# Kernel optimization log

Hardware: AMD Instinct MI355X
Metric: run time of the kernel (lower is better)

The kernel has to match this reference:

```python
import jax, jax.numpy as jnp
import numpy as np

DEGREE = 3
NUM_POINTS = 1024
EPS = 1e-5


def jacobi_kan(x, coeffs, a=1.0, b=1.0, degree=DEGREE):
    # x: (B, C_in, N) -> y: (B, C_out, N)
    t = jnp.tanh(jnp.transpose(x, (0, 2, 1)))  # (B, N, C_in)
    polys = [jnp.ones_like(t)]
    if degree > 0:
        polys.append((a - b + (a + b + 2.0) * t) / 2.0)
    for i in range(2, degree + 1):
        A = (2 * i + a + b - 1) * (2 * i + a + b) / (2 * i * (i + a + b))
        B = (2 * i + a + b - 1) * (a ** 2 - b ** 2) / (2 * i * (i + a + b) * (2 * i + a + b - 2))
        C = -2 * (i + a - 1) * (i + b - 1) * (2 * i + a + b) / (2 * i * (i + a + b) * (2 * i + a + b - 2))
        polys.append((A * t + B) * polys[-1] + C * polys[-2])
    jac = jnp.stack(polys, axis=-1)  # (B, N, C_in, D+1)
    return jnp.einsum('bnid,iod->bon', jac, coeffs)


def batchnorm(x):
    # x: (B, C, N); training-mode BN with batch stats, gamma=1, beta=0
    m = jnp.mean(x, axis=(0, 2), keepdims=True)
    v = jnp.var(x, axis=(0, 2), keepdims=True)
    return (x - m) * jax.lax.rsqrt(v + EPS)


def setup_inputs() -> dict:
    key = jax.random.key(0)
    ks = jax.random.split(key, 11)
    dims = [(2, 64), (64, 64), (64, 64), (64, 128), (128, 1024),
            (1088, 512), (512, 256), (256, 128), (128, 128), (128, 3)]
    inp = {"x": jax.random.normal(ks[0], (32, 2, NUM_POINTS), dtype=jnp.float32)}
    for idx, (i, o) in enumerate(dims):
        std = 1.0 / (i * (DEGREE + 1))
        inp[f"w{idx+1}"] = std * jax.random.normal(ks[idx + 1], (i, o, DEGREE + 1), dtype=jnp.float32)
    return inp


def reference(x, w1, w2, w3, w4, w5, w6, w7, w8, w9, w10):
    h = batchnorm(jacobi_kan(x, w1))
    h = batchnorm(jacobi_kan(h, w2))
    local_feature = h                                  # (B, 64, N)
    h = batchnorm(jacobi_kan(h, w3))
    h = batchnorm(jacobi_kan(h, w4))
    h = batchnorm(jacobi_kan(h, w5))                   # (B, 1024, N)
    gf = jnp.max(h, axis=2, keepdims=True)             # (B, 1024, 1)
    gf = jnp.broadcast_to(gf, (h.shape[0], h.shape[1], NUM_POINTS))
    h = jnp.concatenate([local_feature, gf], axis=1)   # (B, 1088, N)
    h = batchnorm(jacobi_kan(h, w6))
    h = batchnorm(jacobi_kan(h, w7))
    h = batchnorm(jacobi_kan(h, w8))
    h = batchnorm(jacobi_kan(h, w9))
    return jacobi_kan(h, w10)                          # (B, 3, N)
```

## Files before the change

kernel.cpp:

```cpp
#include <hip/hip_runtime.h>

#define BATCH 32
#define NPTS  1024
#define NTOT  (BATCH * NPTS)

typedef _Float16 half8  __attribute__((ext_vector_type(8)));
typedef _Float16 half4v __attribute__((ext_vector_type(4)));
typedef float    f32x4  __attribute__((ext_vector_type(4)));


__device__ __forceinline__ float fast_tanh(float x) {
  float ax = fabsf(x);
  float e  = __expf(-2.0f * ax);
  float t  = (1.0f - e) / (1.0f + e);
  return x < 0.0f ? -t : t;
}

__device__ __forceinline__ void jacobi4(float t, float& p0, float& p1, float& p2, float& p3) {
  float t2 = t * t;
  p0 = 1.0f;
  p1 = 2.0f * t;
  p2 = 3.75f * t2 - 0.75f;
  p3 = t * (7.0f * t2 - 3.0f);
}

__device__ __forceinline__ unsigned encf(float f) {
  unsigned b = __float_as_uint(f);
  return b ^ ((unsigned)((int)b >> 31) | 0x80000000u);
}
__device__ __forceinline__ float decf(unsigned u) {
  unsigned b = (u & 0x80000000u) ? (u ^ 0x80000000u) : ~u;
  return __uint_as_float(b);
}

__global__ void zero_ws(unsigned* __restrict__ p, int n) {
  int i = blockIdx.x * 256 + threadIdx.x;
  if (i < n) p[i] = 0u;
}

__global__ void conv_w16(const float* __restrict__ w, half8* __restrict__ wh,
                         int C_in, int C_out, int BN) {
  const int nslot = C_in >> 1;
  int tid = blockIdx.x * 256 + threadIdx.x;
  int oL = tid % BN;
  int r  = tid / BN;
  int s  = r % nslot;
  int ot = r / nslot;
  int i  = s << 1;
  int o  = ot * BN + oL;
  const float4 wa = *(const float4*)(w + (((size_t)i * C_out + o) << 2));
  const float4 wb = *(const float4*)(w + (((size_t)(i + 1) * C_out + o) << 2));
  half8 h;
  h[0] = (_Float16)(wa.x * 64.0f); h[1] = (_Float16)(wa.y * 64.0f);
  h[2] = (_Float16)(wa.z * 64.0f); h[3] = (_Float16)(wa.w * 64.0f);
  h[4] = (_Float16)(wb.x * 64.0f); h[5] = (_Float16)(wb.y * 64.0f);
  h[6] = (_Float16)(wb.z * 64.0f); h[7] = (_Float16)(wb.w * 64.0f);
  wh[tid] = h;
}

__global__ __launch_bounds__(256) void act_tanh(
    float* y, const float2* __restrict__ st, int C)
{
  size_t i = (((size_t)blockIdx.x << 8) + threadIdx.x) << 2;
  int c = (int)((i >> 10) % (unsigned)C);
  float2 s = st[c];
  float4 v = *(float4*)(y + i);
  v.x = fast_tanh((v.x - s.x) * s.y);
  v.y = fast_tanh((v.y - s.x) * s.y);
  v.z = fast_tanh((v.z - s.x) * s.y);
  v.w = fast_tanh((v.w - s.x) * s.y);
  *(float4*)(y + i) = v;
}

template<int NBW>
__global__ __launch_bounds__(NBW * 128, 2) void kan_mfma3(
    const float* __restrict__ T,
    const half8* __restrict__ wh,
    const float* __restrict__ bias,
    float*       __restrict__ out,
    float2*      __restrict__ spart,
    float*       __restrict__ stat_acc,
    unsigned*    __restrict__ max_acc,
    int C_in, int C_out)
{
  constexpr int BN = NBW * 64;
  const int nslot = C_in >> 1;
  __shared__ float sredS[BN][2], sredS2[BN][2], sredM[BN][2];

  const int t    = threadIdx.x;
  const int lane = t & 63;
  const int col  = lane & 15;
  const int quad = lane >> 4;
  const int wv   = t >> 6;
  const int wm   = wv & 1;
  const int wn   = wv >> 1;
  const int b    = blockIdx.x >> 3;
  const int n0   = (blockIdx.x & 7) << 7;
  const int o0   = blockIdx.y * BN;

  f32x4 acc[4][4];
#pragma unroll
  for (int i = 0; i < 4; ++i)
#pragma unroll
    for (int j = 0; j < 4; ++j)
#pragma unroll
      for (int k = 0; k < 4; ++k) acc[i][j][k] = 0.0f;

  const float* Tp = T + (((size_t)(b * C_in + (quad << 1))) << 10) + n0 + (wm << 6) + col;
  const half8* Bp = wh + (size_t)blockIdx.y * nslot * BN + (size_t)quad * BN + wn * 64 + col;

  for (int s4 = 0; s4 < nslot; s4 += 4) {
    float t0[4], t1[4];
    half8 bf[4];
#pragma unroll
    for (int f = 0; f < 4; ++f) {
      t0[f] = Tp[f << 4];
      t1[f] = Tp[(f << 4) + 1024];
      bf[f] = Bp[f << 4];
    }
    Tp += (size_t)8 << 10;
    Bp += (size_t)4 * BN;
    half8 af[4];
#pragma unroll
    for (int f = 0; f < 4; ++f) {
      float a = t0[f], c = t1[f];
      float as = a * a, cs = c * c;
      half8 h;
      h[0] = (_Float16)1.0f;
      h[1] = (_Float16)(a + a);
      h[2] = (_Float16)(3.75f * as - 0.75f);
      h[3] = (_Float16)(a * (7.0f * as - 3.0f));
      h[4] = (_Float16)1.0f;
      h[5] = (_Float16)(c + c);
      h[6] = (_Float16)(3.75f * cs - 0.75f);
      h[7] = (_Float16)(c * (7.0f * cs - 3.0f));
      af[f] = h;
    }
#pragma unroll
    for (int fm = 0; fm < 4; ++fm)
#pragma unroll
      for (int fn = 0; fn < 4; ++fn)
        acc[fm][fn] = __builtin_amdgcn_mfma_f32_16x16x32_f16(af[fm], bf[fn], acc[fm][fn], 0, 0, 0);
  }

  const float inv64 = 0.015625f;
#pragma unroll
  for (int fn = 0; fn < 4; ++fn) {
    const int cl = (wn << 6) + (fn << 4) + col;
    const int o  = o0 + cl;
    const float bb = bias ? bias[b * C_out + o] : 0.0f;
    float s = 0.f, s2 = 0.f, mx = -3.4e38f;
#pragma unroll
    for (int fm = 0; fm < 4; ++fm) {
      float v0 = acc[fm][fn][0] * inv64 + bb;
      float v1 = acc[fm][fn][1] * inv64 + bb;
      float v2 = acc[fm][fn][2] * inv64 + bb;
      float v3 = acc[fm][fn][3] * inv64 + bb;
      if (out) {
        *(float4*)(out + (((size_t)(b * C_out + o)) << 10) + n0 + (wm << 6) + (fm << 4) + (quad << 2)) =
            make_float4(v0, v1, v2, v3);
      }
      s  += v0 + v1 + v2 + v3;
      s2 += v0 * v0 + v1 * v1 + v2 * v2 + v3 * v3;
      mx  = fmaxf(fmaxf(v0, v1), fmaxf(fmaxf(v2, v3), mx));
    }
    s  += __shfl_down(s, 32);  s  += __shfl_down(s, 16);
    s2 += __shfl_down(s2, 32); s2 += __shfl_down(s2, 16);
    mx  = fmaxf(mx, __shfl_down(mx, 32)); mx = fmaxf(mx, __shfl_down(mx, 16));
    if (lane < 16) {
      sredS [cl][wm] = s;
      sredS2[cl][wm] = s2;
      sredM [cl][wm] = mx;
    }
  }
  __syncthreads();
  if (t < BN) {
    const int o = o0 + t;
    float s  = sredS [t][0] + sredS [t][1];
    float s2 = sredS2[t][0] + sredS2[t][1];
    if (out) {
      spart[(o << 8) + blockIdx.x] = make_float2(s, s2);
    } else {
      float mx = fmaxf(sredM[t][0], sredM[t][1]);
      atomicAdd(&stat_acc[o], s);
      atomicAdd(&stat_acc[C_out + o], s2);
      atomicMax(&max_acc[b * C_out + o], encf(mx));
    }
  }
}

template<int BM, int BN>
__global__ __launch_bounds__(256) void kan_gemm(
    const float*  __restrict__ in, const float2* __restrict__ stats,
    const float*  __restrict__ w, float* __restrict__ out,
    float2* __restrict__ spart, int C_in, int C_out)
{
  static_assert(BM * BN == 256 * 64, "8x8-per-thread tile requires BM*BN == 16384");
  constexpr int TM = BM / 8;
  constexpr int AE = 8 * BM / 256;
  constexpr int BE = 8 * BN / 256;
  __shared__ __align__(16) float As[32][BM];
  __shared__ __align__(16) float Bs[32][BN];

  const int t  = threadIdx.x;
  const int tpb = NPTS / BM;
  const int b  = blockIdx.x / tpb;
  const int n0 = (blockIdx.x % tpb) * BM;
  const int o0 = blockIdx.y * BN;
  const int tm = t % TM;
  const int to = t / TM;

  float acc[2][4][2][4];
#pragma unroll
  for (int a = 0; a < 2; ++a)
#pragma unroll
    for (int c = 0; c < 4; ++c)
#pragma unroll
      for (int d = 0; d < 2; ++d)
#pragma unroll
        for (int e = 0; e < 4; ++e) acc[a][c][d][e] = 0.0f;

  const int nch = (C_in + 7) >> 3;
  for (int ch = 0; ch < nch; ++ch) {
    const int i0 = ch << 3;
    __syncthreads();
#pragma unroll
    for (int r = 0; r < AE; ++r) {
      int e  = t + (r << 8);
      int il = e / BM, n = e % BM;
      int i  = i0 + il;
      float p0 = 0.f, p1 = 0.f, p2 = 0.f, p3 = 0.f;
      if (i < C_in) {
        float v = in[((size_t)(b * C_in + i) << 10) + n0 + n];
        if (stats) { float2 s = stats[i]; v = (v - s.x) * s.y; }
        jacobi4(fast_tanh(v), p0, p1, p2, p3);
      }
      As[(il << 2) + 0][n] = p0;
      As[(il << 2) + 1][n] = p1;
      As[(il << 2) + 2][n] = p2;
      As[(il << 2) + 3][n] = p3;
    }
#pragma unroll
    for (int r = 0; r < BE; ++r) {
      int e  = t + (r << 8);
      int il = e / BN, o = e % BN;
      int i  = i0 + il;
      float4 wv = make_float4(0.f, 0.f, 0.f, 0.f);
      if (i < C_in) wv = *(const float4*)(w + (((size_t)i * C_out + o0 + o) << 2));
      Bs[(il << 2) + 0][o] = wv.x;
      Bs[(il << 2) + 1][o] = wv.y;
      Bs[(il << 2) + 2][o] = wv.z;
      Bs[(il << 2) + 3][o] = wv.w;
    }
    __syncthreads();
#pragma unroll 8
    for (int k = 0; k < 32; ++k) {
      const float4 a0 = *(const float4*)&As[k][tm << 2];
      const float4 a1 = *(const float4*)&As[k][(BM / 2) + (tm << 2)];
      const float4 b0 = *(const float4*)&Bs[k][to << 2];
      const float4 b1 = *(const float4*)&Bs[k][(BN / 2) + (to << 2)];
      const float am[2][4] = {{a0.x, a0.y, a0.z, a0.w}, {a1.x, a1.y, a1.z, a1.w}};
      const float bo[2][4] = {{b0.x, b0.y, b0.z, b0.w}, {b1.x, b1.y, b1.z, b1.w}};
#pragma unroll
      for (int oh = 0; oh < 2; ++oh)
#pragma unroll
        for (int oj = 0; oj < 4; ++oj) {
          const float bv = bo[oh][oj];
#pragma unroll
          for (int mh = 0; mh < 2; ++mh)
#pragma unroll
            for (int mj = 0; mj < 4; ++mj)
              acc[oh][oj][mh][mj] = fmaf(bv, am[mh][mj], acc[oh][oj][mh][mj]);
        }
    }
  }

#pragma unroll
  for (int oh = 0; oh < 2; ++oh)
#pragma unroll
    for (int oj = 0; oj < 4; ++oj) {
      const int o = o0 + oh * (BN / 2) + (to << 2) + oj;
      float s = 0.f, s2 = 0.f;
#pragma unroll
      for (int mh = 0; mh < 2; ++mh) {
        float4 v = make_float4(acc[oh][oj][mh][0], acc[oh][oj][mh][1],
                               acc[oh][oj][mh][2], acc[oh][oj][mh][3]);
        *(float4*)(out + (((size_t)(b * C_out + o)) << 10) + n0 + mh * (BM / 2) + (tm << 2)) = v;
        s  += v.x + v.y + v.z + v.w;
        s2 += v.x * v.x + v.y * v.y + v.z * v.z + v.w * v.w;
      }
#pragma unroll
      for (int off = TM / 2; off > 0; off >>= 1) {
        s  += __shfl_down(s, off, TM);
        s2 += __shfl_down(s2, off, TM);
      }
      if (tm == 0) spart[(o << 8) + blockIdx.x] = make_float2(s, s2);
    }
}

__global__ __launch_bounds__(256) void bn_finalize2(
    const float2* __restrict__ spart, float2* __restrict__ stats, int C, int nxb)
{
  int c = blockIdx.x, t = threadIdx.x;
  float s = 0.f, s2 = 0.f;
  if (t < nxb) { float2 p = spart[(c << 8) + t]; s = p.x; s2 = p.y; }
#pragma unroll
  for (int off = 32; off > 0; off >>= 1) {
    s  += __shfl_down(s, off);
    s2 += __shfl_down(s2, off);
  }
  __shared__ float rs[4], rs2[4];
  int wid = t >> 6;
  if ((t & 63) == 0) { rs[wid] = s; rs2[wid] = s2; }
  __syncthreads();
  if (t == 0) {
    s  = rs[0] + rs[1] + rs[2] + rs[3];
    s2 = rs2[0] + rs2[1] + rs2[2] + rs2[3];
    float m   = s * (1.0f / NTOT);
    float var = s2 * (1.0f / NTOT) - m * m;
    stats[c] = make_float2(m, rsqrtf(var + 1e-5f));
  }
}

__global__ void bn_finalize(const float* __restrict__ stat_acc,
                            float2* __restrict__ stats, int C) {
  int c = blockIdx.x * 256 + threadIdx.x;
  if (c < C) {
    float m   = stat_acc[c] * (1.0f / NTOT);
    float var = stat_acc[C + c] * (1.0f / NTOT) - m * m;
    stats[c] = make_float2(m, rsqrtf(var + 1e-5f));
  }
}

__global__ __launch_bounds__(256) void pool_const6p(
    const unsigned* __restrict__ max_acc, const float2* __restrict__ stats5,
    const float* __restrict__ w6, float* __restrict__ cst)
{
  __shared__ __align__(16) float4 P[32][64];
  const int t  = threadIdx.x;
  const int ot = blockIdx.x;
  const int c0 = blockIdx.y << 6;
#pragma unroll
  for (int it = 0; it < 8; ++it) {
    int idx = t + (it << 8);
    int b = idx >> 6, cl = idx & 63;
    int c = c0 + cl;
    float mx = decf(max_acc[(b << 10) + c]);
    float2 s = stats5[c];
    float tt = fast_tanh((mx - s.x) * s.y);
    float p0, p1, p2, p3; jacobi4(tt, p0, p1, p2, p3);
    P[b][cl] = make_float4(p0, p1, p2, p3);
  }
  __syncthreads();
  const int oL = t & 63;
  const int bg = t >> 6;
  const int o  = (ot << 6) + oL;
  float acc[8];
#pragma unroll
  for (int i = 0; i < 8; ++i) acc[i] = 0.f;
  for (int cl = 0; cl < 64; ++cl) {
    const float4 wv = *(const float4*)(w6 + (((size_t)(64 + c0 + cl) * 512 + o) << 2));
#pragma unroll
    for (int bb = 0; bb < 8; ++bb) {
      float4 p = P[(bg << 3) + bb][cl];
      acc[bb] += p.x * wv.x + p.y * wv.y + p.z * wv.z + p.w * wv.w;
    }
  }
#pragma unroll
  for (int bb = 0; bb < 8; ++bb)
    atomicAdd(&cst[(((bg << 3) + bb) << 9) + o], acc[bb]);
}

__global__ __launch_bounds__(256) void kan_final(
    const float* __restrict__ in, const float2* __restrict__ stats,
    const float* __restrict__ w, float* __restrict__ out)
{
  int g = blockIdx.x * 256 + threadIdx.x;
  int b = g >> 10, n = g & 1023;
  float a0 = 0.f, a1 = 0.f, a2 = 0.f;
  for (int i = 0; i < 128; ++i) {
    float v = in[((size_t)(b * 128 + i) << 10) + n];
    float2 s = stats[i];
    float p0, p1, p2, p3; jacobi4(fast_tanh((v - s.x) * s.y), p0, p1, p2, p3);
    const float4 w0 = *(const float4*)(w + ((i * 3 + 0) << 2));
    const float4 w1 = *(const float4*)(w + ((i * 3 + 1) << 2));
    const float4 w2 = *(const float4*)(w + ((i * 3 + 2) << 2));
    a0 += p0 * w0.x + p1 * w0.y + p2 * w0.z + p3 * w0.w;
    a1 += p0 * w1.x + p1 * w1.y + p2 * w1.z + p3 * w1.w;
    a2 += p0 * w2.x + p1 * w2.y + p2 * w2.z + p3 * w2.w;
  }
  out[((b * 3 + 0) << 10) + n] = a0;
  out[((b * 3 + 1) << 10) + n] = a1;
  out[((b * 3 + 2) << 10) + n] = a2;
}

extern "C" void kernel_launch(void* const* d_in, const int* in_sizes, int n_in,
                              void* d_out, int out_size, void* d_ws, size_t ws_size,
                              hipStream_t stream) {
  const float* x   = (const float*)d_in[0];
  const float* w1  = (const float*)d_in[1];
  const float* w2  = (const float*)d_in[2];
  const float* w3  = (const float*)d_in[3];
  const float* w4  = (const float*)d_in[4];
  const float* w5  = (const float*)d_in[5];
  const float* w6  = (const float*)d_in[6];
  const float* w7  = (const float*)d_in[7];
  const float* w8  = (const float*)d_in[8];
  const float* w9  = (const float*)d_in[9];
  const float* w10 = (const float*)d_in[10];

  float* ws = (float*)d_ws;
  float*    stat_acc = ws + 0;
  unsigned* maxenc   = (unsigned*)(ws + 2048);
  float*    cst6     = ws + 34816;
  float2*   spart    = (float2*)(ws + 51200);
  float2*   stats1   = (float2*)(ws + 313344);
  float2*   stats2   = stats1 + 64;
  float2*   stats3   = stats2 + 64;
  float2*   stats4   = stats3 + 64;
  float2*   stats5   = stats4 + 128;
  float2*   stats6   = stats5 + 1024;
  float2*   stats7   = stats6 + 512;
  float2*   stats8   = stats7 + 256;
  float2*   stats9   = stats8 + 128;
  half8*    whbase = (half8*)(ws + 318464);
  half8*    h2 = whbase + 0;
  half8*    h3 = whbase + 2048;
  half8*    h4 = whbase + 4096;
  half8*    h5 = whbase + 8192;
  half8*    h6 = whbase + 73728;
  half8*    h7 = whbase + 90112;
  half8*    h8 = whbase + 155648;
  half8*    h9 = whbase + 172032;
  float* P   = ws + 1048576;
  float* yT2 = P;
  float* y6  = P + 2097152;
  float* y1  = P + 2097152;
  float* y3  = P + 4194304;
  float* y4  = P + 6291456;
  float* y8  = P + 2097152;
  float* y9  = P + 6291456;
  float* y7  = P + 18874368;

  dim3 blk(256);
  zero_ws<<<200, blk, 0, stream>>>((unsigned*)ws, 51200);
  conv_w16<<<8,   blk, 0, stream>>>(w2, h2, 64, 64, 64);
  conv_w16<<<8,   blk, 0, stream>>>(w3, h3, 64, 64, 64);
  conv_w16<<<16,  blk, 0, stream>>>(w4, h4, 64, 128, 128);
  conv_w16<<<256, blk, 0, stream>>>(w5, h5, 128, 1024, 128);
  conv_w16<<<64,  blk, 0, stream>>>(w6, h6, 64, 512, 128);
  conv_w16<<<256, blk, 0, stream>>>(w7, h7, 512, 256, 128);
  conv_w16<<<64,  blk, 0, stream>>>(w8, h8, 256, 128, 128);
  conv_w16<<<32,  blk, 0, stream>>>(w9, h9, 128, 128, 128);

  kan_gemm<256, 64><<<dim3(128, 1), blk, 0, stream>>>(x, nullptr, w1, y1, spart, 2, 64);
  bn_finalize2<<<64, blk, 0, stream>>>(spart, stats1, 64, 128);
  act_tanh<<<32 * 64, blk, 0, stream>>>(y1, stats1, 64);
  kan_mfma3<1><<<dim3(256, 1), 128, 0, stream>>>(y1, h2, nullptr, yT2, spart, nullptr, nullptr, 64, 64);
  bn_finalize2<<<64, blk, 0, stream>>>(spart, stats2, 64, 256);
  act_tanh<<<32 * 64, blk, 0, stream>>>(yT2, stats2, 64);
  kan_mfma3<1><<<dim3(256, 1), 128, 0, stream>>>(yT2, h3, nullptr, y3, spart, nullptr, nullptr, 64, 64);
  bn_finalize2<<<64, blk, 0, stream>>>(spart, stats3, 64, 256);
  act_tanh<<<32 * 64, blk, 0, stream>>>(y3, stats3, 64);
  kan_mfma3<2><<<dim3(256, 1), blk, 0, stream>>>(y3, h4, nullptr, y4, spart, nullptr, nullptr, 64, 128);
  bn_finalize2<<<128, blk, 0, stream>>>(spart, stats4, 128, 256);
  act_tanh<<<32 * 128, blk, 0, stream>>>(y4, stats4, 128);
  kan_mfma3<2><<<dim3(256, 8), blk, 0, stream>>>(y4, h5, nullptr, nullptr, nullptr, stat_acc, maxenc, 128, 1024);
  bn_finalize<<<4, blk, 0, stream>>>(stat_acc, stats5, 1024);
  pool_const6p<<<dim3(8, 16), blk, 0, stream>>>(maxenc, stats5, w6, cst6);
  kan_mfma3<2><<<dim3(256, 4), blk, 0, stream>>>(yT2, h6, cst6, y6, spart, nullptr, nullptr, 64, 512);
  bn_finalize2<<<512, blk, 0, stream>>>(spart, stats6, 512, 256);
  act_tanh<<<32 * 512, blk, 0, stream>>>(y6, stats6, 512);
  kan_mfma3<2><<<dim3(256, 2), blk, 0, stream>>>(y6, h7, nullptr, y7, spart, nullptr, nullptr, 512, 256);
  bn_finalize2<<<256, blk, 0, stream>>>(spart, stats7, 256, 256);
  act_tanh<<<32 * 256, blk, 0, stream>>>(y7, stats7, 256);
  kan_mfma3<2><<<dim3(256, 1), blk, 0, stream>>>(y7, h8, nullptr, y8, spart, nullptr, nullptr, 256, 128);
  bn_finalize2<<<128, blk, 0, stream>>>(spart, stats8, 128, 256);
  act_tanh<<<32 * 128, blk, 0, stream>>>(y8, stats8, 128);
  kan_mfma3<2><<<dim3(256, 1), blk, 0, stream>>>(y8, h9, nullptr, y9, spart, nullptr, nullptr, 128, 128);
  bn_finalize2<<<128, blk, 0, stream>>>(spart, stats9, 128, 256);
  kan_final<<<128, blk, 0, stream>>>(y9, stats9, w10, (float*)d_out);
}
```

Baseline: 421.3 us.

## Precompute fp16 Jacobi basis per layer and stream it into MFMA GEMMs

Measured after the change: 487.8 us. 1.16x slower.

```diff
diff --git a/kernel.cpp b/kernel.cpp
--- a/kernel.cpp
+++ b/kernel.cpp
@@ -5,7 +5,6 @@
 #define NTOT  (BATCH * NPTS)
 
 typedef _Float16 half8  __attribute__((ext_vector_type(8)));
-typedef _Float16 half4v __attribute__((ext_vector_type(4)));
 typedef float    f32x4  __attribute__((ext_vector_type(4)));
 
 
@@ -58,6 +57,35 @@
   wh[tid] = h;
 }
 
+__global__ __launch_bounds__(256) void act_poly(
+    const float* __restrict__ y, const float2* __restrict__ st,
+    half8* __restrict__ PA, int nslot)
+{
+  int tid = blockIdx.x * 256 + threadIdx.x;
+  int n   = tid & 1023;
+  int r   = tid >> 10;
+  int s   = r % nslot;
+  int b   = r / nslot;
+  int c0  = s << 1;
+  const int C = nslot << 1;
+  float va = y[(((size_t)(b * C + c0)) << 10) + n];
+  float vc = y[(((size_t)(b * C + c0 + 1)) << 10) + n];
+  float2 s0 = st[c0], s1 = st[c0 + 1];
+  float a = fast_tanh((va - s0.x) * s0.y);
+  float c = fast_tanh((vc - s1.x) * s1.y);
+  float as = a * a, cs = c * c;
+  half8 h;
+  h[0] = (_Float16)1.0f;
+  h[1] = (_Float16)(a + a);
+  h[2] = (_Float16)(3.75f * as - 0.75f);
+  h[3] = (_Float16)(a * (7.0f * as - 3.0f));
+  h[4] = (_Float16)1.0f;
+  h[5] = (_Float16)(c + c);
+  h[6] = (_Float16)(3.75f * cs - 0.75f);
+  h[7] = (_Float16)(c * (7.0f * cs - 3.0f));
+  PA[((size_t)r << 10) + n] = h;
+}
+
 __global__ __launch_bounds__(256) void act_tanh(
     float* y, const float2* __restrict__ st, int C)
 {
@@ -72,9 +100,10 @@
   *(float4*)(y + i) = v;
 }
 
-template<int NBW>
-__global__ __launch_bounds__(NBW * 128, 2) void kan_mfma3(
+template<int NBW, bool PRE>
+__global__ __launch_bounds__(NBW * 128, 2) void kan_mfma4(
     const float* __restrict__ T,
+    const half8* __restrict__ PA,
     const half8* __restrict__ wh,
     const float* __restrict__ bias,
     float*       __restrict__ out,
@@ -106,35 +135,45 @@
 #pragma unroll
       for (int k = 0; k < 4; ++k) acc[i][j][k] = 0.0f;
 
-  const float* Tp = T + (((size_t)(b * C_in + (quad << 1))) << 10) + n0 + (wm << 6) + col;
+  const float* Tp = T  + (((size_t)(b * C_in + (quad << 1))) << 10) + n0 + (wm << 6) + col;
+  const half8* Ap = PA + (((size_t)(b * nslot + quad)) << 10) + n0 + (wm << 6) + col;
   const half8* Bp = wh + (size_t)blockIdx.y * nslot * BN + (size_t)quad * BN + wn * 64 + col;
 
   for (int s4 = 0; s4 < nslot; s4 += 4) {
-    float t0[4], t1[4];
-    half8 bf[4];
-#pragma unroll
-    for (int f = 0; f < 4; ++f) {
-      t0[f] = Tp[f << 4];
-      t1[f] = Tp[(f << 4) + 1024];
-      bf[f] = Bp[f << 4];
-    }
-    Tp += (size_t)8 << 10;
-    Bp += (size_t)4 * BN;
-    half8 af[4];
-#pragma unroll
-    for (int f = 0; f < 4; ++f) {
-      float a = t0[f], c = t1[f];
-      float as = a * a, cs = c * c;
-      half8 h;
-      h[0] = (_Float16)1.0f;
-      h[1] = (_Float16)(a + a);
-      h[2] = (_Float16)(3.75f * as - 0.75f);
-      h[3] = (_Float16)(a * (7.0f * as - 3.0f));
-      h[4] = (_Float16)1.0f;
-      h[5] = (_Float16)(c + c);
-      h[6] = (_Float16)(3.75f * cs - 0.75f);
-      h[7] = (_Float16)(c * (7.0f * cs - 3.0f));
-      af[f] = h;
+    half8 af[4], bf[4];
+    if (PRE) {
+#pragma unroll
+      for (int f = 0; f < 4; ++f) {
+        af[f] = Ap[f << 4];
+        bf[f] = Bp[f << 4];
+      }
+      Ap += (size_t)4 << 10;
+      Bp += (size_t)4 * BN;
+    } else {
+      float t0[4], t1[4];
+#pragma unroll
+      for (int f = 0; f < 4; ++f) {
+        t0[f] = Tp[f << 4];
+        t1[f] = Tp[(f << 4) + 1024];
+        bf[f] = Bp[f << 4];
+      }
+      Tp += (size_t)8 << 10;
+      Bp += (size_t)4 * BN;
+#pragma unroll
+      for (int f = 0; f < 4; ++f) {
+        float a = t0[f], c = t1[f];
+        float as = a * a, cs = c * c;
+        half8 h;
+        h[0] = (_Float16)1.0f;
+        h[1] = (_Float16)(a + a);
+        h[2] = (_Float16)(3.75f * as - 0.75f);
+        h[3] = (_Float16)(a * (7.0f * as - 3.0f));
+        h[4] = (_Float16)1.0f;
+        h[5] = (_Float16)(c + c);
+        h[6] = (_Float16)(3.75f * cs - 0.75f);
+        h[7] = (_Float16)(c * (7.0f * cs - 3.0f));
+        af[f] = h;
+      }
     }
 #pragma unroll
     for (int fm = 0; fm < 4; ++fm)
@@ -372,22 +411,25 @@
 }
 
 __global__ __launch_bounds__(256) void kan_final(
-    const float* __restrict__ in, const float2* __restrict__ stats,
-    const float* __restrict__ w, float* __restrict__ out)
+    const half8* __restrict__ PA, const float* __restrict__ w, float* __restrict__ out)
 {
   int g = blockIdx.x * 256 + threadIdx.x;
   int b = g >> 10, n = g & 1023;
   float a0 = 0.f, a1 = 0.f, a2 = 0.f;
-  for (int i = 0; i < 128; ++i) {
-    float v = in[((size_t)(b * 128 + i) << 10) + n];
-    float2 s = stats[i];
-    float p0, p1, p2, p3; jacobi4(fast_tanh((v - s.x) * s.y), p0, p1, p2, p3);
-    const float4 w0 = *(const float4*)(w + ((i * 3 + 0) << 2));
-    const float4 w1 = *(const float4*)(w + ((i * 3 + 1) << 2));
-    const float4 w2 = *(const float4*)(w + ((i * 3 + 2) << 2));
-    a0 += p0 * w0.x + p1 * w0.y + p2 * w0.z + p3 * w0.w;
-    a1 += p0 * w1.x + p1 * w1.y + p2 * w1.z + p3 * w1.w;
-    a2 += p0 * w2.x + p1 * w2.y + p2 * w2.z + p3 * w2.w;
+  for (int s = 0; s < 64; ++s) {
+    half8 h = PA[(((size_t)(b * 64 + s)) << 10) + n];
+#pragma unroll
+    for (int half_i = 0; half_i < 2; ++half_i) {
+      int i = (s << 1) + half_i;
+      float p0 = (float)h[half_i * 4 + 0], p1 = (float)h[half_i * 4 + 1];
+      float p2 = (float)h[half_i * 4 + 2], p3 = (float)h[half_i * 4 + 3];
+      const float4 w0 = *(const float4*)(w + ((i * 3 + 0) << 2));
+      const float4 w1 = *(const float4*)(w + ((i * 3 + 1) << 2));
+      const float4 w2 = *(const float4*)(w + ((i * 3 + 2) << 2));
+      a0 += p0 * w0.x + p1 * w0.y + p2 * w0.z + p3 * w0.w;
+      a1 += p0 * w1.x + p1 * w1.y + p2 * w1.z + p3 * w1.w;
+      a2 += p0 * w2.x + p1 * w2.y + p2 * w2.z + p3 * w2.w;
+    }
   }
   out[((b * 3 + 0) << 10) + n] = a0;
   out[((b * 3 + 1) << 10) + n] = a1;
@@ -432,15 +474,20 @@
   half8*    h7 = whbase + 90112;
   half8*    h8 = whbase + 155648;
   half8*    h9 = whbase + 172032;
-  float* P   = ws + 1048576;
-  float* yT2 = P;
-  float* y6  = P + 2097152;
-  float* y1  = P + 2097152;
-  float* y3  = P + 4194304;
-  float* y4  = P + 6291456;
-  float* y8  = P + 2097152;
-  float* y9  = P + 6291456;
-  float* y7  = P + 18874368;
+  float* P  = ws + 1048576;
+  float* Yv = P;
+  float* PB = P + 4194304;
+  float* PC = P + 12582912;
+  float* PD = P + 16777216;
+  half8* PA1 = (half8*)PB;
+  half8* PA2 = (half8*)PC;
+  half8* PA3 = (half8*)PB;
+  half8* PA4 = (half8*)PB;
+  float* y7  = PB;
+  half8* PA7 = (half8*)PD;
+  half8* PA8 = (half8*)PB;
+  half8* PA9 = (half8*)PB;
+  float* y6  = PD;
 
   dim3 blk(256);
   zero_ws<<<200, blk, 0, stream>>>((unsigned*)ws, 51200);
@@ -453,31 +500,32 @@
   conv_w16<<<64,  blk, 0, stream>>>(w8, h8, 256, 128, 128);
   conv_w16<<<32,  blk, 0, stream>>>(w9, h9, 128, 128, 128);
 
-  kan_gemm<256, 64><<<dim3(128, 1), blk, 0, stream>>>(x, nullptr, w1, y1, spart, 2, 64);
+  kan_gemm<256, 64><<<dim3(128, 1), blk, 0, stream>>>(x, nullptr, w1, Yv, spart, 2, 64);
   bn_finalize2<<<64, blk, 0, stream>>>(spart, stats1, 64, 128);
-  act_tanh<<<32 * 64, blk, 0, stream>>>(y1, stats1, 64);
-  kan_mfma3<1><<<dim3(256, 1), 128, 0, stream>>>(y1, h2, nullptr, yT2, spart, nullptr, nullptr, 64, 64);
+  act_poly<<<128 * 32, blk, 0, stream>>>(Yv, stats1, PA1, 32);
+  kan_mfma4<1, true><<<dim3(256, 1), 128, 0, stream>>>(nullptr, PA1, h2, nullptr, Yv, spart, nullptr, nullptr, 64, 64);
   bn_finalize2<<<64, blk, 0, stream>>>(spart, stats2, 64, 256);
-  act_tanh<<<32 * 64, blk, 0, stream>>>(yT2, stats2, 64);
-  kan_mfma3<1><<<dim3(256, 1), 128, 0, stream>>>(yT2, h3, nullptr, y3, spart, nullptr, nullptr, 64, 64);
+  act_poly<<<128 * 32, blk, 0, stream>>>(Yv, stats2, PA2, 32);
+  kan_mfma4<1, true><<<dim3(256, 1), 128, 0, stream>>>(nullptr, PA2, h3, nullptr, Yv, spart, nullptr, nullptr, 64, 64);
   bn_finalize2<<<64, blk, 0, stream>>>(spart, stats3, 64, 256);
-  act_tanh<<<32 * 64, blk, 0, stream>>>(y3, stats3, 64);
-  kan_mfma3<2><<<dim3(256, 1), blk, 0, stream>>>(y3, h4, nullptr, y4, spart, nullptr, nullptr, 64, 128);
+  act_poly<<<128 * 32, blk, 0, stream>>>(Yv, stats3, PA3, 32);
+  kan_mfma4<2, true><<<dim3(256, 1), blk, 0, stream>>>(nullptr, PA3, h4, nullptr, Yv, spart, nullptr, nullptr, 64, 128);
   bn_finalize2<<<128, blk, 0, stream>>>(spart, stats4, 128, 256);
-  act_tanh<<<32 * 128, blk, 0, stream>>>(y4, stats4, 128);
-  kan_mfma3<2><<<dim3(256, 8), blk, 0, stream>>>(y4, h5, nullptr, nullptr, nullptr, stat_acc, maxenc, 128, 1024);
+  act_poly<<<128 * 64, blk, 0, stream>>>(Yv, stats4, PA4, 64);
+  kan_mfma4<2, true><<<dim3(256, 8), blk, 0, stream>>>(nullptr, PA4, h5, nullptr, nullptr, nullptr, stat_acc, maxenc, 128, 1024);
   bn_finalize<<<4, blk, 0, stream>>>(stat_acc, stats5, 1024);
   pool_const6p<<<dim3(8, 16), blk, 0, stream>>>(maxenc, stats5, w6, cst6);
-  kan_mfma3<2><<<dim3(256, 4), blk, 0, stream>>>(yT2, h6, cst6, y6, spart, nullptr, nullptr, 64, 512);
+  kan_mfma4<2, true><<<dim3(256, 4), blk, 0, stream>>>(nullptr, PA2, h6, cst6, y6, spart, nullptr, nullptr, 64, 512);
   bn_finalize2<<<512, blk, 0, stream>>>(spart, stats6, 512, 256);
   act_tanh<<<32 * 512, blk, 0, stream>>>(y6, stats6, 512);
-  kan_mfma3<2><<<dim3(256, 2), blk, 0, stream>>>(y6, h7, nullptr, y7, spart, nullptr, nullptr, 512, 256);
+  kan_mfma4<2, false><<<dim3(256, 2), blk, 0, stream>>>(y6, nullptr, h7, nullptr, y7, spart, nullptr, nullptr, 512, 256);
   bn_finalize2<<<256, blk, 0, stream>>>(spart, stats7, 256, 256);
-  act_tanh<<<32 * 256, blk, 0, stream>>>(y7, stats7, 256);
-  kan_mfma3<2><<<dim3(256, 1), blk, 0, stream>>>(y7, h8, nullptr, y8, spart, nullptr, nullptr, 256, 128);
+  act_poly<<<128 * 128, blk, 0, stream>>>(y7, stats7, PA7, 128);
+  kan_mfma4<2, true><<<dim3(256, 1), blk, 0, stream>>>(nullptr, PA7, h8, nullptr, Yv, spart, nullptr, nullptr, 256, 128);
   bn_finalize2<<<128, blk, 0, stream>>>(spart, stats8, 128, 256);
-  act_tanh<<<32 * 128, blk, 0, stream>>>(y8, stats8, 128);
-  kan_mfma3<2><<<dim3(256, 1), blk, 0, stream>>>(y8, h9, nullptr, y9, spart, nullptr, nullptr, 128, 128);
+  act_poly<<<128 * 64, blk, 0, stream>>>(Yv, stats8, PA8, 64);
+  kan_mfma4<2, true><<<dim3(256, 1), blk, 0, stream>>>(nullptr, PA8, h9, nullptr, Yv, spart, nullptr, nullptr, 128, 128);
   bn_finalize2<<<128, blk, 0, stream>>>(spart, stats9, 128, 256);
-  kan_final<<<128, blk, 0, stream>>>(y9, stats9, w10, (float*)d_out);
-}
+  act_poly<<<128 * 64, blk, 0, stream>>>(Yv, stats9, PA9, 64);
+  kan_final<<<128, blk, 0, stream>>>(PA9, w10, (float*)d_out);
+}
```

## Fold BN finalize into tanh activation and template MFMA kernel on M-tile

Applied to the files above, without the earlier changes.

Measured after the change: 481.8 us. +14.4%, slower.

```diff
diff --git a/kernel.cpp b/kernel.cpp
--- a/kernel.cpp
+++ b/kernel.cpp
@@ -5,7 +5,6 @@
 #define NTOT  (BATCH * NPTS)
 
 typedef _Float16 half8  __attribute__((ext_vector_type(8)));
-typedef _Float16 half4v __attribute__((ext_vector_type(4)));
 typedef float    f32x4  __attribute__((ext_vector_type(4)));
 
 
@@ -58,22 +57,36 @@
   wh[tid] = h;
 }
 
-__global__ __launch_bounds__(256) void act_tanh(
-    float* y, const float2* __restrict__ st, int C)
+__global__ __launch_bounds__(256) void act_tanh_ip(
+    float* y, const float2* __restrict__ spart, int C, int nxb)
 {
-  size_t i = (((size_t)blockIdx.x << 8) + threadIdx.x) << 2;
-  int c = (int)((i >> 10) % (unsigned)C);
-  float2 s = st[c];
-  float4 v = *(float4*)(y + i);
-  v.x = fast_tanh((v.x - s.x) * s.y);
-  v.y = fast_tanh((v.y - s.x) * s.y);
-  v.z = fast_tanh((v.z - s.x) * s.y);
-  v.w = fast_tanh((v.w - s.x) * s.y);
-  *(float4*)(y + i) = v;
-}
-
-template<int NBW>
-__global__ __launch_bounds__(NBW * 128, 2) void kan_mfma3(
+  const int bc = blockIdx.x;
+  const int c  = bc % C;
+  const int t  = threadIdx.x;
+  float sa = 0.f, sb = 0.f;
+  if (t < nxb) { float2 p = spart[(c << 8) + t]; sa = p.x; sb = p.y; }
+#pragma unroll
+  for (int off = 32; off > 0; off >>= 1) {
+    sa += __shfl_down(sa, off); sb += __shfl_down(sb, off);
+  }
+  __shared__ float red[4][2];
+  if ((t & 63) == 0) { int w = t >> 6; red[w][0] = sa; red[w][1] = sb; }
+  __syncthreads();
+  sa = red[0][0] + red[1][0] + red[2][0] + red[3][0];
+  sb = red[0][1] + red[1][1] + red[2][1] + red[3][1];
+  const float invN = 1.0f / NTOT;
+  float m = sa * invN;
+  float rs = rsqrtf(sb * invN - m * m + 1e-5f);
+  float4 v = *(float4*)(y + ((size_t)bc << 10) + (t << 2));
+  v.x = fast_tanh((v.x - m) * rs);
+  v.y = fast_tanh((v.y - m) * rs);
+  v.z = fast_tanh((v.z - m) * rs);
+  v.w = fast_tanh((v.w - m) * rs);
+  *(float4*)(y + ((size_t)bc << 10) + (t << 2)) = v;
+}
+
+template<int FM, int NBW>
+__global__ __launch_bounds__(NBW * 128) void kan_mfmaT(
     const float* __restrict__ T,
     const half8* __restrict__ wh,
     const float* __restrict__ bias,
@@ -84,6 +97,8 @@
     int C_in, int C_out)
 {
   constexpr int BN = NBW * 64;
+  constexpr int BM = FM * 32;
+  constexpr int HM = FM * 16;
   const int nslot = C_in >> 1;
   __shared__ float sredS[BN][2], sredS2[BN][2], sredM[BN][2];
 
@@ -94,35 +109,37 @@
   const int wv   = t >> 6;
   const int wm   = wv & 1;
   const int wn   = wv >> 1;
-  const int b    = blockIdx.x >> 3;
-  const int n0   = (blockIdx.x & 7) << 7;
+  constexpr int tpb = 1024 / BM;
+  const int b    = blockIdx.x / tpb;
+  const int n0   = (blockIdx.x % tpb) * BM;
   const int o0   = blockIdx.y * BN;
 
-  f32x4 acc[4][4];
-#pragma unroll
-  for (int i = 0; i < 4; ++i)
+  f32x4 acc[FM][4];
+#pragma unroll
+  for (int i = 0; i < FM; ++i)
 #pragma unroll
     for (int j = 0; j < 4; ++j)
 #pragma unroll
       for (int k = 0; k < 4; ++k) acc[i][j][k] = 0.0f;
 
-  const float* Tp = T + (((size_t)(b * C_in + (quad << 1))) << 10) + n0 + (wm << 6) + col;
+  const float* Tp = T + (((size_t)(b * C_in + (quad << 1))) << 10) + n0 + wm * HM + col;
   const half8* Bp = wh + (size_t)blockIdx.y * nslot * BN + (size_t)quad * BN + wn * 64 + col;
 
   for (int s4 = 0; s4 < nslot; s4 += 4) {
-    float t0[4], t1[4];
+    float t0[FM], t1[FM];
     half8 bf[4];
 #pragma unroll
-    for (int f = 0; f < 4; ++f) {
+    for (int f = 0; f < FM; ++f) {
       t0[f] = Tp[f << 4];
       t1[f] = Tp[(f << 4) + 1024];
-      bf[f] = Bp[f << 4];
-    }
+    }
+#pragma unroll
+    for (int f = 0; f < 4; ++f) bf[f] = Bp[f << 4];
     Tp += (size_t)8 << 10;
     Bp += (size_t)4 * BN;
-    half8 af[4];
-#pragma unroll
-    for (int f = 0; f < 4; ++f) {
+    half8 af[FM];
+#pragma unroll
+    for (int f = 0; f < FM; ++f) {
       float a = t0[f], c = t1[f];
       float as = a * a, cs = c * c;
       half8 h;
@@ -137,7 +154,7 @@
       af[f] = h;
     }
 #pragma unroll
-    for (int fm = 0; fm < 4; ++fm)
+    for (int fm = 0; fm < FM; ++fm)
 #pragma unroll
       for (int fn = 0; fn < 4; ++fn)
         acc[fm][fn] = __builtin_amdgcn_mfma_f32_16x16x32_f16(af[fm], bf[fn], acc[fm][fn], 0, 0, 0);
@@ -151,13 +168,13 @@
     const float bb = bias ? bias[b * C_out + o] : 0.0f;
     float s = 0.f, s2 = 0.f, mx = -3.4e38f;
 #pragma unroll
-    for (int fm = 0; fm < 4; ++fm) {
+    for (int fm = 0; fm < FM; ++fm) {
       float v0 = acc[fm][fn][0] * inv64 + bb;
       float v1 = acc[fm][fn][1] * inv64 + bb;
       float v2 = acc[fm][fn][2] * inv64 + bb;
       float v3 = acc[fm][fn][3] * inv64 + bb;
       if (out) {
-        *(float4*)(out + (((size_t)(b * C_out + o)) << 10) + n0 + (wm << 6) + (fm << 4) + (quad << 2)) =
+        *(float4*)(out + (((size_t)(b * C_out + o)) << 10) + n0 + wm * HM + (fm << 4) + (quad << 2)) =
             make_float4(v0, v1, v2, v3);
       }
       s  += v0 + v1 + v2 + v3;
@@ -298,30 +315,6 @@
     }
 }
 
-__global__ __launch_bounds__(256) void bn_finalize2(
-    const float2* __restrict__ spart, float2* __restrict__ stats, int C, int nxb)
-{
-  int c = blockIdx.x, t = threadIdx.x;
-  float s = 0.f, s2 = 0.f;
-  if (t < nxb) { float2 p = spart[(c << 8) + t]; s = p.x; s2 = p.y; }
-#pragma unroll
-  for (int off = 32; off > 0; off >>= 1) {
-    s  += __shfl_down(s, off);
-    s2 += __shfl_down(s2, off);
-  }
-  __shared__ float rs[4], rs2[4];
-  int wid = t >> 6;
-  if ((t & 63) == 0) { rs[wid] = s; rs2[wid] = s2; }
-  __syncthreads();
-  if (t == 0) {
-    s  = rs[0] + rs[1] + rs[2] + rs[3];
-    s2 = rs2[0] + rs2[1] + rs2[2] + rs2[3];
-    float m   = s * (1.0f / NTOT);
-    float var = s2 * (1.0f / NTOT) - m * m;
-    stats[c] = make_float2(m, rsqrtf(var + 1e-5f));
-  }
-}
-
 __global__ void bn_finalize(const float* __restrict__ stat_acc,
                             float2* __restrict__ stats, int C) {
   int c = blockIdx.x * 256 + threadIdx.x;
@@ -372,16 +365,14 @@
 }
 
 __global__ __launch_bounds__(256) void kan_final(
-    const float* __restrict__ in, const float2* __restrict__ stats,
-    const float* __restrict__ w, float* __restrict__ out)
+    const float* __restrict__ tin, const float* __restrict__ w, float* __restrict__ out)
 {
   int g = blockIdx.x * 256 + threadIdx.x;
   int b = g >> 10, n = g & 1023;
   float a0 = 0.f, a1 = 0.f, a2 = 0.f;
   for (int i = 0; i < 128; ++i) {
-    float v = in[((size_t)(b * 128 + i) << 10) + n];
-    float2 s = stats[i];
-    float p0, p1, p2, p3; jacobi4(fast_tanh((v - s.x) * s.y), p0, p1, p2, p3);
+    float tt = tin[((size_t)(b * 128 + i) << 10) + n];
+    float p0, p1, p2, p3; jacobi4(tt, p0, p1, p2, p3);
     const float4 w0 = *(const float4*)(w + ((i * 3 + 0) << 2));
     const float4 w1 = *(const float4*)(w + ((i * 3 + 1) << 2));
     const float4 w2 = *(const float4*)(w + ((i * 3 + 2) << 2));
@@ -414,15 +405,7 @@
   unsigned* maxenc   = (unsigned*)(ws + 2048);
   float*    cst6     = ws + 34816;
   float2*   spart    = (float2*)(ws + 51200);
-  float2*   stats1   = (float2*)(ws + 313344);
-  float2*   stats2   = stats1 + 64;
-  float2*   stats3   = stats2 + 64;
-  float2*   stats4   = stats3 + 64;
-  float2*   stats5   = stats4 + 128;
-  float2*   stats6   = stats5 + 1024;
-  float2*   stats7   = stats6 + 512;
-  float2*   stats8   = stats7 + 256;
-  float2*   stats9   = stats8 + 128;
+  float2*   stats5   = (float2*)(ws + 313344);
   half8*    whbase = (half8*)(ws + 318464);
   half8*    h2 = whbase + 0;
   half8*    h3 = whbase + 2048;
@@ -432,15 +415,18 @@
   half8*    h7 = whbase + 90112;
   half8*    h8 = whbase + 155648;
   half8*    h9 = whbase + 172032;
-  float* P   = ws + 1048576;
-  float* yT2 = P;
-  float* y6  = P + 2097152;
-  float* y1  = P + 2097152;
-  float* y3  = P + 4194304;
-  float* y4  = P + 6291456;
-  float* y8  = P + 2097152;
-  float* y9  = P + 6291456;
-  float* y7  = P + 18874368;
+  float* P  = ws + 1048576;
+  float* A  = P;
+  float* B  = P + 16777216;
+  float* C  = P + 18874368;
+  float* y1 = A;
+  float* y3 = A;
+  float* y4 = A + 2097152;
+  float* y6 = A;
+  float* y8 = A;
+  float* y9 = A + 4194304;
+  float* y2 = B;
+  float* y7 = C;
 
   dim3 blk(256);
   zero_ws<<<200, blk, 0, stream>>>((unsigned*)ws, 51200);
@@ -454,30 +440,23 @@
   conv_w16<<<32,  blk, 0, stream>>>(w9, h9, 128, 128, 128);
 
   kan_gemm<256, 64><<<dim3(128, 1), blk, 0, stream>>>(x, nullptr, w1, y1, spart, 2, 64);
-  bn_finalize2<<<64, blk, 0, stream>>>(spart, stats1, 64, 128);
-  act_tanh<<<32 * 64, blk, 0, stream>>>(y1, stats1, 64);
-  kan_mfma3<1><<<dim3(256, 1), 128, 0, stream>>>(y1, h2, nullptr, yT2, spart, nullptr, nullptr, 64, 64);
-  bn_finalize2<<<64, blk, 0, stream>>>(spart, stats2, 64, 256);
-  act_tanh<<<32 * 64, blk, 0, stream>>>(yT2, stats2, 64);
-  kan_mfma3<1><<<dim3(256, 1), 128, 0, stream>>>(yT2, h3, nullptr, y3, spart, nullptr, nullptr, 64, 64);
-  bn_finalize2<<<64, blk, 0, stream>>>(spart, stats3, 64, 256);
-  act_tanh<<<32 * 64, blk, 0, stream>>>(y3, stats3, 64);
-  kan_mfma3<2><<<dim3(256, 1), blk, 0, stream>>>(y3, h4, nullptr, y4, spart, nullptr, nullptr, 64, 128);
-  bn_finalize2<<<128, blk, 0, stream>>>(spart, stats4, 128, 256);
-  act_tanh<<<32 * 128, blk, 0, stream>>>(y4, stats4, 128);
-  kan_mfma3<2><<<dim3(256, 8), blk, 0, stream>>>(y4, h5, nullptr, nullptr, nullptr, stat_acc, maxenc, 128, 1024);
+  act_tanh_ip<<<32 * 64, blk, 0, stream>>>(y1, spart, 64, 128);
+  kan_mfmaT<4, 1><<<dim3(256, 1), 128, 0, stream>>>(y1, h2, nullptr, y2, spart, nullptr, nullptr, 64, 64);
+  act_tanh_ip<<<32 * 64, blk, 0, stream>>>(y2, spart, 64, 256);
+  kan_mfmaT<4, 1><<<dim3(256, 1), 128, 0, stream>>>(y2, h3, nullptr, y3, spart, nullptr, nullptr, 64, 64);
+  act_tanh_ip<<<32 * 64, blk, 0, stream>>>(y3, spart, 64, 256);
+  kan_mfmaT<4, 2><<<dim3(256, 1), blk, 0, stream>>>(y3, h4, nullptr, y4, spart, nullptr, nullptr, 64, 128);
+  act_tanh_ip<<<32 * 128, blk, 0, stream>>>(y4, spart, 128, 256);
+  kan_mfmaT<8, 2><<<dim3(128, 8), blk, 0, stream>>>(y4, h5, nullptr, nullptr, nullptr, stat_acc, maxenc, 128, 1024);
   bn_finalize<<<4, blk, 0, stream>>>(stat_acc, stats5, 1024);
   pool_const6p<<<dim3(8, 16), blk, 0, stream>>>(maxenc, stats5, w6, cst6);
-  kan_mfma3<2><<<dim3(256, 4), blk, 0, stream>>>(yT2, h6, cst6, y6, spart, nullptr, nullptr, 64, 512);
-  bn_finalize2<<<512, blk, 0, stream>>>(spart, stats6, 512, 256);
-  act_tanh<<<32 * 512, blk, 0, stream>>>(y6, stats6, 512);
-  kan_mfma3<2><<<dim3(256, 2), blk, 0, stream>>>(y6, h7, nullptr, y7, spart, nullptr, nullptr, 512, 256);
-  bn_finalize2<<<256, blk, 0, stream>>>(spart, stats7, 256, 256);
-  act_tanh<<<32 * 256, blk, 0, stream>>>(y7, stats7, 256);
-  kan_mfma3<2><<<dim3(256, 1), blk, 0, stream>>>(y7, h8, nullptr, y8, spart, nullptr, nullptr, 256, 128);
-  bn_finalize2<<<128, blk, 0, stream>>>(spart, stats8, 128, 256);
-  act_tanh<<<32 * 128, blk, 0, stream>>>(y8, stats8, 128);
-  kan_mfma3<2><<<dim3(256, 1), blk, 0, stream>>>(y8, h9, nullptr, y9, spart, nullptr, nullptr, 128, 128);
-  bn_finalize2<<<128, blk, 0, stream>>>(spart, stats9, 128, 256);
-  kan_final<<<128, blk, 0, stream>>>(y9, stats9, w10, (float*)d_out);
-}
+  kan_mfmaT<8, 2><<<dim3(128, 4), blk, 0, stream>>>(y2, h6, cst6, y6, spart, nullptr, nullptr, 64, 512);
+  act_tanh_ip<<<32 * 512, blk, 0, stream>>>(y6, spart, 512, 128);
+  kan_mfmaT<8, 2><<<dim3(128, 2), blk, 0, stream>>>(y6, h7, nullptr, y7, spart, nullptr, nullptr, 512, 256);
+  act_tanh_ip<<<32 * 256, blk, 0, stream>>>(y7, spart, 256, 128);
+  kan_mfmaT<4, 2><<<dim3(256, 1), blk, 0, stream>>>(y7, h8, nullptr, y8, spart, nullptr, nullptr, 256, 128);
+  act_tanh_ip<<<32 * 128, blk, 0, stream>>>(y8, spart, 128, 256);
+  kan_mfmaT<4, 2><<<dim3(256, 1), blk, 0, stream>>>(y8, h9, nullptr, y9, spart, nullptr, nullptr, 128, 128);
+  act_tanh_ip<<<32 * 128, blk, 0, stream>>>(y9, spart, 128, 256);
+  kan_final<<<128, blk, 0, stream>>>(y9, w10, (float*)d_out);
+}
```
